# Kernel optimization log

Measured on AMD Instinct MI355X. Metric: run time of the kernel, lower is better.

The kernel has to match this reference:

```python
import jax, jax.numpy as jnp
import numpy as np

EPS = 1e-10

def setup_inputs() -> dict:
    key = jax.random.key(0)
    k1, k2 = jax.random.split(key)
    B, N, D = 8, 4096, 3
    points_ref = jax.random.normal(k1, (B, N, D), dtype=jnp.float32)
    points = jax.random.normal(k2, (B, N, D), dtype=jnp.float32)
    return {"points_ref": points_ref, "points": points, "nn_size": 16}

def _knn(points_ref, K):
    # pairwise squared distances (B,N,N)
    sq = jnp.sum(points_ref * points_ref, axis=-1)
    d2 = sq[:, :, None] + sq[:, None, :] - 2.0 * jnp.einsum('bnd,bmd->bnm', points_ref, points_ref)
    _, idx = jax.lax.top_k(-d2, K)  # nearest first; idx: (B,N,K)
    return idx

def reference(points_ref, points, nn_size):
    K = nn_size + 1
    knn_idx = _knn(points_ref, K)[:, :, 1:]  # drop self -> (B,N,nn_size)
    gather = jax.vmap(lambda p, i: p[i])  # (N,D),(N,K) -> (N,K,D)
    group_ref = gather(points_ref, knn_idx)           # (B,N,K,D)
    group_pred = gather(points, knn_idx)              # (B,N,K,D)
    dist_ref = jnp.linalg.norm(group_ref - points_ref[:, :, None, :], axis=-1)  # (B,N,K)
    dist = jnp.linalg.norm(group_pred - points[:, :, None, :], axis=-1)         # (B,N,K)
    stretch = jnp.maximum(dist / (dist_ref + EPS) - 1.0, 0.0)
    return jnp.mean(stretch)
```

## Files before the change

### kernel.cpp

```cpp
#include <hip/hip_runtime.h>

#define NPTS  4096
#define KNN   16
#define K1    17
#define NBLK  64
#define CELLS 4096
#define GQ    2
#define EPSF  1e-10f

__device__ __forceinline__ unsigned umin_(unsigned a, unsigned b) { return a < b ? a : b; }
__device__ __forceinline__ unsigned umax_(unsigned a, unsigned b) { return a < b ? b : a; }
__device__ __forceinline__ unsigned rdlane(unsigned v, int l) {
    return (unsigned)__builtin_amdgcn_readlane((int)v, l);
}

#define DPP_XOR1(v)  ((unsigned)__builtin_amdgcn_update_dpp(0, (int)(v), 0xB1, 0xF, 0xF, true))
#define DPP_XOR2(v)  ((unsigned)__builtin_amdgcn_update_dpp(0, (int)(v), 0x4E, 0xF, 0xF, true))
#define SWZ_XOR(v,J) ((unsigned)__builtin_amdgcn_ds_swizzle((int)(v), ((J) << 10) | 0x1F))
#define DPP_SHR1(v)  ((unsigned)__builtin_amdgcn_update_dpp(0, (int)(v), 0x111, 0xF, 0xF, true))
#define DPPF_SHR(vf, CTRL) __uint_as_float((unsigned)__builtin_amdgcn_update_dpp(0, (int)__float_as_uint(vf), CTRL, 0xF, 0xF, true))
#define LXOR1(v)  DPP_XOR1(v)
#define LXOR2(v)  DPP_XOR2(v)
#define LXOR4(v)  SWZ_XOR(v, 4)
#define LXOR8(v)  SWZ_XOR(v, 8)
#define LXOR16(v) SWZ_XOR(v, 16)
#define LXOR32(v) ((unsigned)__shfl_xor((int)(v), 32))

#define BSTEP(K, XORF) do {                                                   \
    unsigned o1_ = XORF(arr), o2_ = XORF(bk);                                 \
    bool tm_ = (((lane & (J_)) == 0) == ((lane & (K)) == 0));                 \
    unsigned mn1_ = umin_(arr, o1_), mx1_ = umax_(arr, o1_);                  \
    unsigned mn2_ = umin_(bk, o2_),  mx2_ = umax_(bk, o2_);                   \
    arr = tm_ ? mn1_ : mx1_; bk = tm_ ? mn2_ : mx2_;                          \
} while (0)

__device__ __forceinline__ unsigned sp4(int v) {
    unsigned x = (unsigned)v;
    return (x & 1u) | ((x & 2u) << 2) | ((x & 4u) << 4) | ((x & 8u) << 6);
}

__global__ __launch_bounds__(1024) void sort_kernel(
    const float* __restrict__ pref,
    float4* __restrict__ wxyzw, int* __restrict__ widx, float4* __restrict__ wbb)
{
    __shared__ unsigned hist[CELLS];
    __shared__ unsigned short cells[NPTS];
    __shared__ unsigned wofs[16];
    const int tid  = threadIdx.x;
    const int lane = tid & 63, w = tid >> 6;
    const int b = blockIdx.x;
    const float* prb = pref + (size_t)b * NPTS * 3;
    const size_t base = (size_t)b * NPTS;

    for (int t = tid; t < CELLS; t += 1024) hist[t] = 0u;
    __syncthreads();

    for (int p = tid; p < NPTS; p += 1024) {
        float x = prb[3 * p + 0], y = prb[3 * p + 1], z = prb[3 * p + 2];
        int cx = min(15, max(0, (int)((x + 4.0f) * 2.0f)));
        int cy = min(15, max(0, (int)((y + 4.0f) * 2.0f)));
        int cz = min(15, max(0, (int)((z + 4.0f) * 2.0f)));
        unsigned m = sp4(cx) | (sp4(cy) << 1) | (sp4(cz) << 2);
        cells[p] = (unsigned short)m;
        atomicAdd(&hist[m], 1u);
    }
    __syncthreads();

    unsigned l0 = hist[4 * tid + 0], l1 = hist[4 * tid + 1];
    unsigned l2 = hist[4 * tid + 2], l3 = hist[4 * tid + 3];
    unsigned s = l0 + l1 + l2 + l3;
    unsigned run = s;
#pragma unroll
    for (int d = 1; d < 64; d <<= 1) {
        unsigned o = __shfl_up(run, d);
        if (lane >= d) run += o;
    }
    if (lane == 63) wofs[w] = run;
    __syncthreads();
    if (tid == 0) {
        unsigned acc = 0;
#pragma unroll
        for (int k = 0; k < 16; ++k) { unsigned t2 = wofs[k]; wofs[k] = acc; acc += t2; }
    }
    __syncthreads();
    unsigned excl = wofs[w] + run - s;
    hist[4 * tid + 0] = excl;
    hist[4 * tid + 1] = excl + l0;
    hist[4 * tid + 2] = excl + l0 + l1;
    hist[4 * tid + 3] = excl + l0 + l1 + l2;
    __syncthreads();

    for (int p = tid; p < NPTS; p += 1024) {
        unsigned c = cells[p];
        unsigned pos = atomicAdd(&hist[c], 1u);
        wxyzw[base + pos] = make_float4(prb[3 * p + 0], prb[3 * p + 1], prb[3 * p + 2], 0.f);
        widx[base + pos]  = p;
    }
    __syncthreads();

#pragma unroll
    for (int rep = 0; rep < 4; ++rep) {
        int blk = w + rep * 16;
        float4 c = wxyzw[base + blk * 64 + lane];
        float mnx = c.x, mxx = c.x, mny = c.y, mxy2 = c.y, mnz = c.z, mxz = c.z;
#pragma unroll
        for (int d = 32; d > 0; d >>= 1) {
            mnx  = fminf(mnx,  __shfl_xor(mnx,  d));
            mxx  = fmaxf(mxx,  __shfl_xor(mxx,  d));
            mny  = fminf(mny,  __shfl_xor(mny,  d));
            mxy2 = fmaxf(mxy2, __shfl_xor(mxy2, d));
            mnz  = fminf(mnz,  __shfl_xor(mnz,  d));
            mxz  = fmaxf(mxz,  __shfl_xor(mxz,  d));
        }
        if (lane == 0) {
            wbb[((size_t)b * NBLK + blk) * 2 + 0] = make_float4(mnx, mny, mnz, 0.f);
            wbb[((size_t)b * NBLK + blk) * 2 + 1] = make_float4(mxx, mxy2, mxz, 0.f);
        }
    }
}

#define EVENTS(KEY) do {                                                      \
    unsigned long long m_ = __ballot((KEY) < thr);                            \
    if (m_) {                                                                 \
        do {                                                                  \
            int l_ = __ffsll(m_) - 1;                                         \
            m_ &= m_ - 1;                                                     \
            unsigned kk_ = rdlane(KEY, l_);                                   \
            unsigned long long lt_ = __ballot(arr < kk_) & 0x1FFFFull;        \
            int pos_ = __popcll(lt_);                                         \
            unsigned up_ = DPP_SHR1(arr);                                     \
            unsigned a15_ = rdlane(arr, 15);                                  \
            up_ = (lane == 16) ? a15_ : up_;                                  \
            arr = (lane == pos_) ? kk_ : ((lane > pos_) ? up_ : arr);         \
        } while (m_);                                                         \
        thr = rdlane(arr, K1 - 1);                                            \
    } } while (0)

__global__ __launch_bounds__(256, 8) void knn_main_kernel(
    const float* __restrict__ ppred,
    const float4* __restrict__ wxyzw, const int* __restrict__ widx,
    const float4* __restrict__ wbb, float* __restrict__ partials, int NQ)
{
    const int lane = threadIdx.x & 63;
    const int wv   = blockIdx.x * 4 + (threadIdx.x >> 6);
    const bool pow2 = (NQ & (NQ - 1)) == 0;

#pragma unroll 1
    for (int t = 0; t < GQ; ++t) {
        const int qid = wv * GQ + t;
        const int q = pow2 ? (int)(((unsigned)qid * 26765u) & (unsigned)(NQ - 1)) : qid;

        const int b = q >> 12;
        const int p = q & (NPTS - 1);
        const size_t base = (size_t)b * NPTS;
        const int p0 = p & ~63, ownblk = p >> 6;

        const float4 qc = wxyzw[base + p];
        const float qx = qc.x, qy = qc.y, qz = qc.z;

        unsigned arr;
        {
            float4 c = wxyzw[base + p0 + lane];
            float dx = c.x - qx, dy = c.y - qy, dz = c.z - qz;
            float d2 = dx * dx + dy * dy + dz * dz;
            arr = (__float_as_uint(d2) & 0xFFFFF000u) | (unsigned)(p0 + lane);
        }
        unsigned bk;
        {
            float4 mn4 = wbb[((size_t)b * NBLK + lane) * 2 + 0];
            float4 mx4 = wbb[((size_t)b * NBLK + lane) * 2 + 1];
            float ddx = fmaxf(fmaxf(mn4.x - qx, qx - mx4.x), 0.0f);
            float ddy = fmaxf(fmaxf(mn4.y - qy, qy - mx4.y), 0.0f);
            float ddz = fmaxf(fmaxf(mn4.z - qz, qz - mx4.z), 0.0f);
            float bd2 = ddx * ddx + ddy * ddy + ddz * ddz;
            bk = (__float_as_uint(bd2) & 0xFFFFF000u) | (unsigned)lane;
            bk = (lane == ownblk) ? 0xFFFFFFFFu : bk;
        }

        {
            int J_;
            J_ = 1;  BSTEP(2,  LXOR1);
            J_ = 2;  BSTEP(4,  LXOR2);  J_ = 1; BSTEP(4,  LXOR1);
            J_ = 4;  BSTEP(8,  LXOR4);  J_ = 2; BSTEP(8,  LXOR2);  J_ = 1; BSTEP(8,  LXOR1);
            J_ = 8;  BSTEP(16, LXOR8);  J_ = 4; BSTEP(16, LXOR4);  J_ = 2; BSTEP(16, LXOR2);  J_ = 1; BSTEP(16, LXOR1);
            J_ = 16; BSTEP(32, LXOR16); J_ = 8; BSTEP(32, LXOR8);  J_ = 4; BSTEP(32, LXOR4);  J_ = 2; BSTEP(32, LXOR2); J_ = 1; BSTEP(32, LXOR1);
            J_ = 32; BSTEP(64, LXOR32); J_ = 16; BSTEP(64, LXOR16); J_ = 8; BSTEP(64, LXOR8); J_ = 4; BSTEP(64, LXOR4); J_ = 2; BSTEP(64, LXOR2); J_ = 1; BSTEP(64, LXOR1);
        }
        unsigned thr = rdlane(arr, K1 - 1);

        int k = 0;
        unsigned bcur = rdlane(bk, 0);
        bool have = (bcur < thr);
        float4 cur;
        if (have) cur = wxyzw[base + (int)(bcur & 0xFFFu) * 64 + lane];
        while (have) {
            unsigned bnext = rdlane(bk, k + 1);
            bool pf = (bnext < thr);
            float4 nxt;
            if (pf) nxt = wxyzw[base + (int)(bnext & 0xFFFu) * 64 + lane];
            int jbase = (int)(bcur & 0xFFFu) * 64;
            float dx = cur.x - qx, dy = cur.y - qy, dz = cur.z - qz;
            float d2 = dx * dx + dy * dy + dz * dz;
            unsigned key = (__float_as_uint(d2) & 0xFFFFF000u) | (unsigned)(jbase + lane);
            EVENTS(key);
            ++k;
            bcur = bnext;
            have = (bcur < thr);
            cur = nxt;
        }

        const float* ppb = ppred + (size_t)b * NPTS * 3;
        const int iorig = widx[base + p];
        float s = 0.f;
        if (lane >= 1 && lane <= KNN) {
            int js = (int)(arr & 0xFFFu);
            float4 rc = wxyzw[base + js];
            float rx = rc.x - qx, ry = rc.y - qy, rz = rc.z - qz;
            float dref = sqrtf(rx * rx + ry * ry + rz * rz);
            int nj = widx[base + js];
            float px = ppb[3 * iorig + 0], py = ppb[3 * iorig + 1], pz = ppb[3 * iorig + 2];
            float ax = ppb[3 * nj + 0] - px;
            float ay = ppb[3 * nj + 1] - py;
            float az = ppb[3 * nj + 2] - pz;
            float dpred = sqrtf(ax * ax + ay * ay + az * az);
            s = fmaxf(dpred / (dref + EPSF) - 1.0f, 0.0f);
        }
        s += DPPF_SHR(s, 0x111);
        s += DPPF_SHR(s, 0x112);
        s += DPPF_SHR(s, 0x114);
        s += DPPF_SHR(s, 0x118);
        float t15 = __uint_as_float(rdlane(__float_as_uint(s), 15));
        float t16 = __uint_as_float(rdlane(__float_as_uint(s), 16));
        if (lane == 0) partials[q] = t15 + t16;
    }
}

__global__ __launch_bounds__(1024) void reduce_kernel(
    const float* __restrict__ partials, int n, float* __restrict__ out, float scale)
{
    __shared__ float wsum[16];
    float s = 0.f;
    for (int idx = threadIdx.x; idx < n; idx += 1024) s += partials[idx];
    for (int off = 32; off > 0; off >>= 1) s += __shfl_down(s, off);
    if ((threadIdx.x & 63) == 0) wsum[threadIdx.x >> 6] = s;
    __syncthreads();
    if (threadIdx.x == 0) {
        float t = 0.f;
#pragma unroll
        for (int k = 0; k < 16; ++k) t += wsum[k];
        out[0] = t * scale;
    }
}

extern "C" void kernel_launch(void* const* d_in, const int* in_sizes, int n_in,
                              void* d_out, int out_size, void* d_ws, size_t ws_size,
                              hipStream_t stream) {
    const float* pref  = (const float*)d_in[0];
    const float* ppred = (const float*)d_in[1];
    float* out = (float*)d_out;

    const int B  = in_sizes[0] / (NPTS * 3);
    const int NQ = B * NPTS;
    const int nblocks = NQ / (GQ * 4);
    const float scale = 1.0f / ((float)NQ * (float)KNN);

    char* ws = (char*)d_ws;
    float4* wxyzw = (float4*)ws;
    int*    widx  = (int*)   (ws + (size_t)B * NPTS * 16);
    float4* wbb   = (float4*)(ws + (size_t)B * NPTS * 20);
    float*  partials = (float*)(ws + (size_t)B * NPTS * 20 + (size_t)B * NBLK * 32);

    sort_kernel<<<dim3(B), dim3(1024), 0, stream>>>(pref, wxyzw, widx, wbb);
    knn_main_kernel<<<dim3(nblocks), dim3(256), 0, stream>>>(ppred, wxyzw, widx, wbb, partials, NQ);
    reduce_kernel<<<dim3(1), dim3(1024), 0, stream>>>(partials, NQ, out, scale);
}
```

Measured before the change: 77.49 us.

## Seed KNN candidates from own and adjacent block with bitonic merge, one query per wave

Seeds each query's candidate list from two sorted blocks, its own and the XOR-adjacent one, rather than one. It does this by sorting two 64-lane arrays in opposite directions and merging them with a bitonic min-and-clean step. The goal is a tighter initial threshold so fewer blocks have to be scanned in the event loop. It also drops the two-queries-per-wave loop and launches one wave per query, adding blocks for more parallelism at the cost of the extra sort network work per query.

```diff
diff --git a/kernel.cpp b/kernel.cpp
--- a/kernel.cpp
+++ b/kernel.cpp
@@ -5,7 +5,6 @@
 #define K1    17
 #define NBLK  64
 #define CELLS 4096
-#define GQ    2
 #define EPSF  1e-10f
 
 __device__ __forceinline__ unsigned umin_(unsigned a, unsigned b) { return a < b ? a : b; }
@@ -26,12 +25,17 @@
 #define LXOR16(v) SWZ_XOR(v, 16)
 #define LXOR32(v) ((unsigned)__shfl_xor((int)(v), 32))
 
-#define BSTEP(K, XORF) do {                                                   \
-    unsigned o1_ = XORF(arr), o2_ = XORF(bk);                                 \
+#define BSTEP3(K, XORF) do {                                                  \
+    unsigned oa_ = XORF(arrA), ob_ = XORF(arrB), ok_ = XORF(bk);              \
     bool tm_ = (((lane & (J_)) == 0) == ((lane & (K)) == 0));                 \
-    unsigned mn1_ = umin_(arr, o1_), mx1_ = umax_(arr, o1_);                  \
-    unsigned mn2_ = umin_(bk, o2_),  mx2_ = umax_(bk, o2_);                   \
-    arr = tm_ ? mn1_ : mx1_; bk = tm_ ? mn2_ : mx2_;                          \
+    arrA = tm_ ? umin_(arrA, oa_) : umax_(arrA, oa_);                         \
+    arrB = tm_ ? umax_(arrB, ob_) : umin_(arrB, ob_);                         \
+    bk   = tm_ ? umin_(bk,   ok_) : umax_(bk,   ok_);                         \
+} while (0)
+
+#define CSTEP(J, XORF) do {                                                   \
+    unsigned o_ = XORF(arr);                                                  \
+    arr = ((lane & (J)) == 0) ? umin_(arr, o_) : umax_(arr, o_);              \
 } while (0)
 
 __device__ __forceinline__ unsigned sp4(int v) {
@@ -143,96 +147,102 @@
 {
     const int lane = threadIdx.x & 63;
     const int wv   = blockIdx.x * 4 + (threadIdx.x >> 6);
-    const bool pow2 = (NQ & (NQ - 1)) == 0;
-
-#pragma unroll 1
-    for (int t = 0; t < GQ; ++t) {
-        const int qid = wv * GQ + t;
-        const int q = pow2 ? (int)(((unsigned)qid * 26765u) & (unsigned)(NQ - 1)) : qid;
-
-        const int b = q >> 12;
-        const int p = q & (NPTS - 1);
-        const size_t base = (size_t)b * NPTS;
-        const int p0 = p & ~63, ownblk = p >> 6;
-
-        const float4 qc = wxyzw[base + p];
-        const float qx = qc.x, qy = qc.y, qz = qc.z;
-
-        unsigned arr;
-        {
-            float4 c = wxyzw[base + p0 + lane];
-            float dx = c.x - qx, dy = c.y - qy, dz = c.z - qz;
-            float d2 = dx * dx + dy * dy + dz * dz;
-            arr = (__float_as_uint(d2) & 0xFFFFF000u) | (unsigned)(p0 + lane);
-        }
-        unsigned bk;
-        {
-            float4 mn4 = wbb[((size_t)b * NBLK + lane) * 2 + 0];
-            float4 mx4 = wbb[((size_t)b * NBLK + lane) * 2 + 1];
-            float ddx = fmaxf(fmaxf(mn4.x - qx, qx - mx4.x), 0.0f);
-            float ddy = fmaxf(fmaxf(mn4.y - qy, qy - mx4.y), 0.0f);
-            float ddz = fmaxf(fmaxf(mn4.z - qz, qz - mx4.z), 0.0f);
-            float bd2 = ddx * ddx + ddy * ddy + ddz * ddz;
-            bk = (__float_as_uint(bd2) & 0xFFFFF000u) | (unsigned)lane;
-            bk = (lane == ownblk) ? 0xFFFFFFFFu : bk;
-        }
-
-        {
-            int J_;
-            J_ = 1;  BSTEP(2,  LXOR1);
-            J_ = 2;  BSTEP(4,  LXOR2);  J_ = 1; BSTEP(4,  LXOR1);
-            J_ = 4;  BSTEP(8,  LXOR4);  J_ = 2; BSTEP(8,  LXOR2);  J_ = 1; BSTEP(8,  LXOR1);
-            J_ = 8;  BSTEP(16, LXOR8);  J_ = 4; BSTEP(16, LXOR4);  J_ = 2; BSTEP(16, LXOR2);  J_ = 1; BSTEP(16, LXOR1);
-            J_ = 16; BSTEP(32, LXOR16); J_ = 8; BSTEP(32, LXOR8);  J_ = 4; BSTEP(32, LXOR4);  J_ = 2; BSTEP(32, LXOR2); J_ = 1; BSTEP(32, LXOR1);
-            J_ = 32; BSTEP(64, LXOR32); J_ = 16; BSTEP(64, LXOR16); J_ = 8; BSTEP(64, LXOR8); J_ = 4; BSTEP(64, LXOR4); J_ = 2; BSTEP(64, LXOR2); J_ = 1; BSTEP(64, LXOR1);
-        }
-        unsigned thr = rdlane(arr, K1 - 1);
-
-        int k = 0;
-        unsigned bcur = rdlane(bk, 0);
-        bool have = (bcur < thr);
-        float4 cur;
-        if (have) cur = wxyzw[base + (int)(bcur & 0xFFFu) * 64 + lane];
-        while (have) {
-            unsigned bnext = rdlane(bk, k + 1);
-            bool pf = (bnext < thr);
-            float4 nxt;
-            if (pf) nxt = wxyzw[base + (int)(bnext & 0xFFFu) * 64 + lane];
-            int jbase = (int)(bcur & 0xFFFu) * 64;
-            float dx = cur.x - qx, dy = cur.y - qy, dz = cur.z - qz;
-            float d2 = dx * dx + dy * dy + dz * dz;
-            unsigned key = (__float_as_uint(d2) & 0xFFFFF000u) | (unsigned)(jbase + lane);
-            EVENTS(key);
-            ++k;
-            bcur = bnext;
-            have = (bcur < thr);
-            cur = nxt;
-        }
-
-        const float* ppb = ppred + (size_t)b * NPTS * 3;
-        const int iorig = widx[base + p];
-        float s = 0.f;
-        if (lane >= 1 && lane <= KNN) {
-            int js = (int)(arr & 0xFFFu);
-            float4 rc = wxyzw[base + js];
-            float rx = rc.x - qx, ry = rc.y - qy, rz = rc.z - qz;
-            float dref = sqrtf(rx * rx + ry * ry + rz * rz);
-            int nj = widx[base + js];
-            float px = ppb[3 * iorig + 0], py = ppb[3 * iorig + 1], pz = ppb[3 * iorig + 2];
-            float ax = ppb[3 * nj + 0] - px;
-            float ay = ppb[3 * nj + 1] - py;
-            float az = ppb[3 * nj + 2] - pz;
-            float dpred = sqrtf(ax * ax + ay * ay + az * az);
-            s = fmaxf(dpred / (dref + EPSF) - 1.0f, 0.0f);
-        }
-        s += DPPF_SHR(s, 0x111);
-        s += DPPF_SHR(s, 0x112);
-        s += DPPF_SHR(s, 0x114);
-        s += DPPF_SHR(s, 0x118);
-        float t15 = __uint_as_float(rdlane(__float_as_uint(s), 15));
-        float t16 = __uint_as_float(rdlane(__float_as_uint(s), 16));
-        if (lane == 0) partials[q] = t15 + t16;
-    }
+    const int q = ((NQ & (NQ - 1)) == 0) ? (int)(((unsigned)wv * 26765u) & (unsigned)(NQ - 1)) : wv;
+
+    const int b = q >> 12;
+    const int p = q & (NPTS - 1);
+    const size_t base = (size_t)b * NPTS;
+    const int p0 = p & ~63, ownblk = p >> 6;
+    const int adjblk = ownblk ^ 1;
+
+    const float4 qc = wxyzw[base + p];
+    const float qx = qc.x, qy = qc.y, qz = qc.z;
+
+    unsigned arrA, arrB;
+    {
+        float4 c1 = wxyzw[base + p0 + lane];
+        float4 c2 = wxyzw[base + (p0 ^ 64) + lane];
+        float dx = c1.x - qx, dy = c1.y - qy, dz = c1.z - qz;
+        float d2 = dx * dx + dy * dy + dz * dz;
+        arrA = (__float_as_uint(d2) & 0xFFFFF000u) | (unsigned)(p0 + lane);
+        dx = c2.x - qx; dy = c2.y - qy; dz = c2.z - qz;
+        d2 = dx * dx + dy * dy + dz * dz;
+        arrB = (__float_as_uint(d2) & 0xFFFFF000u) | (unsigned)((p0 ^ 64) + lane);
+    }
+    unsigned bk;
+    {
+        float4 mn4 = wbb[((size_t)b * NBLK + lane) * 2 + 0];
+        float4 mx4 = wbb[((size_t)b * NBLK + lane) * 2 + 1];
+        float ddx = fmaxf(fmaxf(mn4.x - qx, qx - mx4.x), 0.0f);
+        float ddy = fmaxf(fmaxf(mn4.y - qy, qy - mx4.y), 0.0f);
+        float ddz = fmaxf(fmaxf(mn4.z - qz, qz - mx4.z), 0.0f);
+        float bd2 = ddx * ddx + ddy * ddy + ddz * ddz;
+        bk = (__float_as_uint(bd2) & 0xFFFFF000u) | (unsigned)lane;
+        bk = (lane == ownblk || lane == adjblk) ? 0xFFFFFFFFu : bk;
+    }
+
+    {
+        int J_;
+        J_ = 1;  BSTEP3(2,  LXOR1);
+        J_ = 2;  BSTEP3(4,  LXOR2);  J_ = 1; BSTEP3(4,  LXOR1);
+        J_ = 4;  BSTEP3(8,  LXOR4);  J_ = 2; BSTEP3(8,  LXOR2);  J_ = 1; BSTEP3(8,  LXOR1);
+        J_ = 8;  BSTEP3(16, LXOR8);  J_ = 4; BSTEP3(16, LXOR4);  J_ = 2; BSTEP3(16, LXOR2);  J_ = 1; BSTEP3(16, LXOR1);
+        J_ = 16; BSTEP3(32, LXOR16); J_ = 8; BSTEP3(32, LXOR8);  J_ = 4; BSTEP3(32, LXOR4);  J_ = 2; BSTEP3(32, LXOR2); J_ = 1; BSTEP3(32, LXOR1);
+        J_ = 32; BSTEP3(64, LXOR32); J_ = 16; BSTEP3(64, LXOR16); J_ = 8; BSTEP3(64, LXOR8); J_ = 4; BSTEP3(64, LXOR4); J_ = 2; BSTEP3(64, LXOR2); J_ = 1; BSTEP3(64, LXOR1);
+    }
+    unsigned arr = umin_(arrA, arrB);
+    CSTEP(32, LXOR32);
+    CSTEP(16, LXOR16);
+    CSTEP(8,  LXOR8);
+    CSTEP(4,  LXOR4);
+    CSTEP(2,  LXOR2);
+    CSTEP(1,  LXOR1);
+    unsigned thr = rdlane(arr, K1 - 1);
+
+    int k = 0;
+    unsigned bcur = rdlane(bk, 0);
+    bool have = (bcur < thr);
+    float4 cur;
+    if (have) cur = wxyzw[base + (int)(bcur & 0xFFFu) * 64 + lane];
+    while (have) {
+        unsigned bnext = rdlane(bk, k + 1);
+        bool pf = (bnext < thr);
+        float4 nxt;
+        if (pf) nxt = wxyzw[base + (int)(bnext & 0xFFFu) * 64 + lane];
+        int jbase = (int)(bcur & 0xFFFu) * 64;
+        float dx = cur.x - qx, dy = cur.y - qy, dz = cur.z - qz;
+        float d2 = dx * dx + dy * dy + dz * dz;
+        unsigned key = (__float_as_uint(d2) & 0xFFFFF000u) | (unsigned)(jbase + lane);
+        EVENTS(key);
+        ++k;
+        bcur = bnext;
+        have = (bcur < thr);
+        cur = nxt;
+    }
+
+    const float* ppb = ppred + (size_t)b * NPTS * 3;
+    const int iorig = widx[base + p];
+    float s = 0.f;
+    if (lane >= 1 && lane <= KNN) {
+        int js = (int)(arr & 0xFFFu);
+        float4 rc = wxyzw[base + js];
+        float rx = rc.x - qx, ry = rc.y - qy, rz = rc.z - qz;
+        float dref = sqrtf(rx * rx + ry * ry + rz * rz);
+        int nj = widx[base + js];
+        float px = ppb[3 * iorig + 0], py = ppb[3 * iorig + 1], pz = ppb[3 * iorig + 2];
+        float ax = ppb[3 * nj + 0] - px;
+        float ay = ppb[3 * nj + 1] - py;
+        float az = ppb[3 * nj + 2] - pz;
+        float dpred = sqrtf(ax * ax + ay * ay + az * az);
+        s = fmaxf(dpred / (dref + EPSF) - 1.0f, 0.0f);
+    }
+    s += DPPF_SHR(s, 0x111);
+    s += DPPF_SHR(s, 0x112);
+    s += DPPF_SHR(s, 0x114);
+    s += DPPF_SHR(s, 0x118);
+    float t15 = __uint_as_float(rdlane(__float_as_uint(s), 15));
+    float t16 = __uint_as_float(rdlane(__float_as_uint(s), 16));
+    if (lane == 0) partials[q] = t15 + t16;
 }
 
 __global__ __launch_bounds__(1024) void reduce_kernel(
@@ -261,7 +271,6 @@
 
     const int B  = in_sizes[0] / (NPTS * 3);
     const int NQ = B * NPTS;
-    const int nblocks = NQ / (GQ * 4);
     const float scale = 1.0f / ((float)NQ * (float)KNN);
 
     char* ws = (char*)d_ws;
@@ -271,6 +280,6 @@
     float*  partials = (float*)(ws + (size_t)B * NPTS * 20 + (size_t)B * NBLK * 32);
 
     sort_kernel<<<dim3(B), dim3(1024), 0, stream>>>(pref, wxyzw, widx, wbb);
-    knn_main_kernel<<<dim3(nblocks), dim3(256), 0, stream>>>(ppred, wxyzw, widx, wbb, partials, NQ);
+    knn_main_kernel<<<dim3(NQ / 4), dim3(256), 0, stream>>>(ppred, wxyzw, widx, wbb, partials, NQ);
     reduce_kernel<<<dim3(1), dim3(1024), 0, stream>>>(partials, NQ, out, scale);
 }
```

Result: faster. 75.68 us (-2.3%).

## Split bbox into own kernel, one query per wave, block-level partial sums

Applied to the files above, without the earlier changes.

Moves the per-block bounding-box reduction out of the 8-block sort kernel into a separate, widely parallel bbox kernel. The main KNN kernel now handles one query per wave instead of two, doubling the grid, and sums each block's partials in shared memory so the final reduction reads a quarter as many values through float4 loads. This trades an extra kernel launch and a block barrier for more parallelism and a shorter serial sort stage.

```diff
diff --git a/kernel.cpp b/kernel.cpp
--- a/kernel.cpp
+++ b/kernel.cpp
@@ -5,7 +5,6 @@
 #define K1    17
 #define NBLK  64
 #define CELLS 4096
-#define GQ    2
 #define EPSF  1e-10f
 
 __device__ __forceinline__ unsigned umin_(unsigned a, unsigned b) { return a < b ? a : b; }
@@ -41,7 +40,7 @@
 
 __global__ __launch_bounds__(1024) void sort_kernel(
     const float* __restrict__ pref,
-    float4* __restrict__ wxyzw, int* __restrict__ widx, float4* __restrict__ wbb)
+    float4* __restrict__ wxyzw, int* __restrict__ widx)
 {
     __shared__ unsigned hist[CELLS];
     __shared__ unsigned short cells[NPTS];
@@ -96,26 +95,31 @@
         wxyzw[base + pos] = make_float4(prb[3 * p + 0], prb[3 * p + 1], prb[3 * p + 2], 0.f);
         widx[base + pos]  = p;
     }
-    __syncthreads();
-
-#pragma unroll
-    for (int rep = 0; rep < 4; ++rep) {
-        int blk = w + rep * 16;
-        float4 c = wxyzw[base + blk * 64 + lane];
-        float mnx = c.x, mxx = c.x, mny = c.y, mxy2 = c.y, mnz = c.z, mxz = c.z;
-#pragma unroll
-        for (int d = 32; d > 0; d >>= 1) {
-            mnx  = fminf(mnx,  __shfl_xor(mnx,  d));
-            mxx  = fmaxf(mxx,  __shfl_xor(mxx,  d));
-            mny  = fminf(mny,  __shfl_xor(mny,  d));
-            mxy2 = fmaxf(mxy2, __shfl_xor(mxy2, d));
-            mnz  = fminf(mnz,  __shfl_xor(mnz,  d));
-            mxz  = fmaxf(mxz,  __shfl_xor(mxz,  d));
-        }
-        if (lane == 0) {
-            wbb[((size_t)b * NBLK + blk) * 2 + 0] = make_float4(mnx, mny, mnz, 0.f);
-            wbb[((size_t)b * NBLK + blk) * 2 + 1] = make_float4(mxx, mxy2, mxz, 0.f);
-        }
+}
+
+__global__ __launch_bounds__(512) void bbox_kernel(
+    const float4* __restrict__ wxyzw, float4* __restrict__ wbb)
+{
+    const int lane = threadIdx.x & 63;
+    const int gb = blockIdx.x * 8 + (threadIdx.x >> 6);
+    const int b  = gb >> 6;
+    const int blk = gb & (NBLK - 1);
+    const size_t base = (size_t)b * NPTS;
+
+    float4 c = wxyzw[base + blk * 64 + lane];
+    float mnx = c.x, mxx = c.x, mny = c.y, mxy2 = c.y, mnz = c.z, mxz = c.z;
+#pragma unroll
+    for (int d = 32; d > 0; d >>= 1) {
+        mnx  = fminf(mnx,  __shfl_xor(mnx,  d));
+        mxx  = fmaxf(mxx,  __shfl_xor(mxx,  d));
+        mny  = fminf(mny,  __shfl_xor(mny,  d));
+        mxy2 = fmaxf(mxy2, __shfl_xor(mxy2, d));
+        mnz  = fminf(mnz,  __shfl_xor(mnz,  d));
+        mxz  = fmaxf(mxz,  __shfl_xor(mxz,  d));
+    }
+    if (lane == 0) {
+        wbb[(size_t)gb * 2 + 0] = make_float4(mnx, mny, mnz, 0.f);
+        wbb[(size_t)gb * 2 + 1] = make_float4(mxx, mxy2, mxz, 0.f);
     }
 }
 
@@ -141,106 +145,111 @@
     const float4* __restrict__ wxyzw, const int* __restrict__ widx,
     const float4* __restrict__ wbb, float* __restrict__ partials, int NQ)
 {
+    __shared__ float wsum[4];
     const int lane = threadIdx.x & 63;
-    const int wv   = blockIdx.x * 4 + (threadIdx.x >> 6);
-    const bool pow2 = (NQ & (NQ - 1)) == 0;
-
-#pragma unroll 1
-    for (int t = 0; t < GQ; ++t) {
-        const int qid = wv * GQ + t;
-        const int q = pow2 ? (int)(((unsigned)qid * 26765u) & (unsigned)(NQ - 1)) : qid;
-
-        const int b = q >> 12;
-        const int p = q & (NPTS - 1);
-        const size_t base = (size_t)b * NPTS;
-        const int p0 = p & ~63, ownblk = p >> 6;
-
-        const float4 qc = wxyzw[base + p];
-        const float qx = qc.x, qy = qc.y, qz = qc.z;
-
-        unsigned arr;
-        {
-            float4 c = wxyzw[base + p0 + lane];
-            float dx = c.x - qx, dy = c.y - qy, dz = c.z - qz;
-            float d2 = dx * dx + dy * dy + dz * dz;
-            arr = (__float_as_uint(d2) & 0xFFFFF000u) | (unsigned)(p0 + lane);
-        }
-        unsigned bk;
-        {
-            float4 mn4 = wbb[((size_t)b * NBLK + lane) * 2 + 0];
-            float4 mx4 = wbb[((size_t)b * NBLK + lane) * 2 + 1];
-            float ddx = fmaxf(fmaxf(mn4.x - qx, qx - mx4.x), 0.0f);
-            float ddy = fmaxf(fmaxf(mn4.y - qy, qy - mx4.y), 0.0f);
-            float ddz = fmaxf(fmaxf(mn4.z - qz, qz - mx4.z), 0.0f);
-            float bd2 = ddx * ddx + ddy * ddy + ddz * ddz;
-            bk = (__float_as_uint(bd2) & 0xFFFFF000u) | (unsigned)lane;
-            bk = (lane == ownblk) ? 0xFFFFFFFFu : bk;
-        }
-
-        {
-            int J_;
-            J_ = 1;  BSTEP(2,  LXOR1);
-            J_ = 2;  BSTEP(4,  LXOR2);  J_ = 1; BSTEP(4,  LXOR1);
-            J_ = 4;  BSTEP(8,  LXOR4);  J_ = 2; BSTEP(8,  LXOR2);  J_ = 1; BSTEP(8,  LXOR1);
-            J_ = 8;  BSTEP(16, LXOR8);  J_ = 4; BSTEP(16, LXOR4);  J_ = 2; BSTEP(16, LXOR2);  J_ = 1; BSTEP(16, LXOR1);
-            J_ = 16; BSTEP(32, LXOR16); J_ = 8; BSTEP(32, LXOR8);  J_ = 4; BSTEP(32, LXOR4);  J_ = 2; BSTEP(32, LXOR2); J_ = 1; BSTEP(32, LXOR1);
-            J_ = 32; BSTEP(64, LXOR32); J_ = 16; BSTEP(64, LXOR16); J_ = 8; BSTEP(64, LXOR8); J_ = 4; BSTEP(64, LXOR4); J_ = 2; BSTEP(64, LXOR2); J_ = 1; BSTEP(64, LXOR1);
-        }
-        unsigned thr = rdlane(arr, K1 - 1);
-
-        int k = 0;
-        unsigned bcur = rdlane(bk, 0);
-        bool have = (bcur < thr);
-        float4 cur;
-        if (have) cur = wxyzw[base + (int)(bcur & 0xFFFu) * 64 + lane];
-        while (have) {
-            unsigned bnext = rdlane(bk, k + 1);
-            bool pf = (bnext < thr);
-            float4 nxt;
-            if (pf) nxt = wxyzw[base + (int)(bnext & 0xFFFu) * 64 + lane];
-            int jbase = (int)(bcur & 0xFFFu) * 64;
-            float dx = cur.x - qx, dy = cur.y - qy, dz = cur.z - qz;
-            float d2 = dx * dx + dy * dy + dz * dz;
-            unsigned key = (__float_as_uint(d2) & 0xFFFFF000u) | (unsigned)(jbase + lane);
-            EVENTS(key);
-            ++k;
-            bcur = bnext;
-            have = (bcur < thr);
-            cur = nxt;
-        }
-
-        const float* ppb = ppred + (size_t)b * NPTS * 3;
-        const int iorig = widx[base + p];
-        float s = 0.f;
-        if (lane >= 1 && lane <= KNN) {
-            int js = (int)(arr & 0xFFFu);
-            float4 rc = wxyzw[base + js];
-            float rx = rc.x - qx, ry = rc.y - qy, rz = rc.z - qz;
-            float dref = sqrtf(rx * rx + ry * ry + rz * rz);
-            int nj = widx[base + js];
-            float px = ppb[3 * iorig + 0], py = ppb[3 * iorig + 1], pz = ppb[3 * iorig + 2];
-            float ax = ppb[3 * nj + 0] - px;
-            float ay = ppb[3 * nj + 1] - py;
-            float az = ppb[3 * nj + 2] - pz;
-            float dpred = sqrtf(ax * ax + ay * ay + az * az);
-            s = fmaxf(dpred / (dref + EPSF) - 1.0f, 0.0f);
-        }
-        s += DPPF_SHR(s, 0x111);
-        s += DPPF_SHR(s, 0x112);
-        s += DPPF_SHR(s, 0x114);
-        s += DPPF_SHR(s, 0x118);
-        float t15 = __uint_as_float(rdlane(__float_as_uint(s), 15));
-        float t16 = __uint_as_float(rdlane(__float_as_uint(s), 16));
-        if (lane == 0) partials[q] = t15 + t16;
-    }
+    const int w    = threadIdx.x >> 6;
+    const int wv   = blockIdx.x * 4 + w;
+    const int q = ((NQ & (NQ - 1)) == 0) ? (int)(((unsigned)wv * 26765u) & (unsigned)(NQ - 1)) : wv;
+
+    const int b = q >> 12;
+    const int p = q & (NPTS - 1);
+    const size_t base = (size_t)b * NPTS;
+    const int p0 = p & ~63, ownblk = p >> 6;
+
+    const float4 qc = wxyzw[base + p];
+    const float qx = qc.x, qy = qc.y, qz = qc.z;
+
+    unsigned arr;
+    {
+        float4 c = wxyzw[base + p0 + lane];
+        float dx = c.x - qx, dy = c.y - qy, dz = c.z - qz;
+        float d2 = dx * dx + dy * dy + dz * dz;
+        arr = (__float_as_uint(d2) & 0xFFFFF000u) | (unsigned)(p0 + lane);
+    }
+    unsigned bk;
+    {
+        float4 mn4 = wbb[((size_t)b * NBLK + lane) * 2 + 0];
+        float4 mx4 = wbb[((size_t)b * NBLK + lane) * 2 + 1];
+        float ddx = fmaxf(fmaxf(mn4.x - qx, qx - mx4.x), 0.0f);
+        float ddy = fmaxf(fmaxf(mn4.y - qy, qy - mx4.y), 0.0f);
+        float ddz = fmaxf(fmaxf(mn4.z - qz, qz - mx4.z), 0.0f);
+        float bd2 = ddx * ddx + ddy * ddy + ddz * ddz;
+        bk = (__float_as_uint(bd2) & 0xFFFFF000u) | (unsigned)lane;
+        bk = (lane == ownblk) ? 0xFFFFFFFFu : bk;
+    }
+
+    {
+        int J_;
+        J_ = 1;  BSTEP(2,  LXOR1);
+        J_ = 2;  BSTEP(4,  LXOR2);  J_ = 1; BSTEP(4,  LXOR1);
+        J_ = 4;  BSTEP(8,  LXOR4);  J_ = 2; BSTEP(8,  LXOR2);  J_ = 1; BSTEP(8,  LXOR1);
+        J_ = 8;  BSTEP(16, LXOR8);  J_ = 4; BSTEP(16, LXOR4);  J_ = 2; BSTEP(16, LXOR2);  J_ = 1; BSTEP(16, LXOR1);
+        J_ = 16; BSTEP(32, LXOR16); J_ = 8; BSTEP(32, LXOR8);  J_ = 4; BSTEP(32, LXOR4);  J_ = 2; BSTEP(32, LXOR2); J_ = 1; BSTEP(32, LXOR1);
+        J_ = 32; BSTEP(64, LXOR32); J_ = 16; BSTEP(64, LXOR16); J_ = 8; BSTEP(64, LXOR8); J_ = 4; BSTEP(64, LXOR4); J_ = 2; BSTEP(64, LXOR2); J_ = 1; BSTEP(64, LXOR1);
+    }
+    unsigned thr = rdlane(arr, K1 - 1);
+
+    int k = 0;
+    unsigned bcur = rdlane(bk, 0);
+    bool have = (bcur < thr);
+    float4 cur;
+    if (have) cur = wxyzw[base + (int)(bcur & 0xFFFu) * 64 + lane];
+    while (have) {
+        unsigned bnext = rdlane(bk, k + 1);
+        bool pf = (bnext < thr);
+        float4 nxt;
+        if (pf) nxt = wxyzw[base + (int)(bnext & 0xFFFu) * 64 + lane];
+        int jbase = (int)(bcur & 0xFFFu) * 64;
+        float dx = cur.x - qx, dy = cur.y - qy, dz = cur.z - qz;
+        float d2 = dx * dx + dy * dy + dz * dz;
+        unsigned key = (__float_as_uint(d2) & 0xFFFFF000u) | (unsigned)(jbase + lane);
+        EVENTS(key);
+        ++k;
+        bcur = bnext;
+        have = (bcur < thr);
+        cur = nxt;
+    }
+
+    const float* ppb = ppred + (size_t)b * NPTS * 3;
+    const int iorig = widx[base + p];
+    float s = 0.f;
+    if (lane >= 1 && lane <= KNN) {
+        int js = (int)(arr & 0xFFFu);
+        float4 rc = wxyzw[base + js];
+        float rx = rc.x - qx, ry = rc.y - qy, rz = rc.z - qz;
+        float dref = sqrtf(rx * rx + ry * ry + rz * rz);
+        int nj = widx[base + js];
+        float px = ppb[3 * iorig + 0], py = ppb[3 * iorig + 1], pz = ppb[3 * iorig + 2];
+        float ax = ppb[3 * nj + 0] - px;
+        float ay = ppb[3 * nj + 1] - py;
+        float az = ppb[3 * nj + 2] - pz;
+        float dpred = sqrtf(ax * ax + ay * ay + az * az);
+        s = fmaxf(dpred / (dref + EPSF) - 1.0f, 0.0f);
+    }
+    s += DPPF_SHR(s, 0x111);
+    s += DPPF_SHR(s, 0x112);
+    s += DPPF_SHR(s, 0x114);
+    s += DPPF_SHR(s, 0x118);
+    float t15 = __uint_as_float(rdlane(__float_as_uint(s), 15));
+    float t16 = __uint_as_float(rdlane(__float_as_uint(s), 16));
+
+    if (lane == 0) wsum[w] = t15 + t16;
+    __syncthreads();
+    if (threadIdx.x == 0)
+        partials[blockIdx.x] = (wsum[0] + wsum[1]) + (wsum[2] + wsum[3]);
 }
 
 __global__ __launch_bounds__(1024) void reduce_kernel(
     const float* __restrict__ partials, int n, float* __restrict__ out, float scale)
 {
     __shared__ float wsum[16];
+    const float4* p4 = (const float4*)partials;
+    const int n4 = n >> 2;
     float s = 0.f;
-    for (int idx = threadIdx.x; idx < n; idx += 1024) s += partials[idx];
+    for (int idx = threadIdx.x; idx < n4; idx += 1024) {
+        float4 v = p4[idx];
+        s += (v.x + v.y) + (v.z + v.w);
+    }
     for (int off = 32; off > 0; off >>= 1) s += __shfl_down(s, off);
     if ((threadIdx.x & 63) == 0) wsum[threadIdx.x >> 6] = s;
     __syncthreads();
@@ -261,7 +270,7 @@
 
     const int B  = in_sizes[0] / (NPTS * 3);
     const int NQ = B * NPTS;
-    const int nblocks = NQ / (GQ * 4);
+    const int nblocks = NQ / 4;
     const float scale = 1.0f / ((float)NQ * (float)KNN);
 
     char* ws = (char*)d_ws;
@@ -270,7 +279,8 @@
     float4* wbb   = (float4*)(ws + (size_t)B * NPTS * 20);
     float*  partials = (float*)(ws + (size_t)B * NPTS * 20 + (size_t)B * NBLK * 32);
 
-    sort_kernel<<<dim3(B), dim3(1024), 0, stream>>>(pref, wxyzw, widx, wbb);
+    sort_kernel<<<dim3(B), dim3(1024), 0, stream>>>(pref, wxyzw, widx);
+    bbox_kernel<<<dim3(B * NBLK / 8), dim3(512), 0, stream>>>(wxyzw, wbb);
     knn_main_kernel<<<dim3(nblocks), dim3(256), 0, stream>>>(ppred, wxyzw, widx, wbb, partials, NQ);
-    reduce_kernel<<<dim3(1), dim3(1024), 0, stream>>>(partials, NQ, out, scale);
-}
+    reduce_kernel<<<dim3(1), dim3(1024), 0, stream>>>(partials, nblocks, out, scale);
+}
```

After: 65.64 us, median of 2. 1.18x faster.
